# Kernel optimization log

Measured on AMD Instinct MI355X. Metric: run time of the kernel, lower is better.

The kernel has to match this reference:

```python
import jax, jax.numpy as jnp
import numpy as np

B, S, D, H = 2, 2048, 1024, 16
DEPTH = D // H


def setup_inputs() -> dict:
    key = jax.random.key(0)
    ks = jax.random.split(key, 12)
    s = 0.02
    inp = {
        "query": jax.random.normal(ks[0], (B, S, D), jnp.float32),
        "key": jax.random.normal(ks[1], (B, S, D), jnp.float32),
        "value": jax.random.normal(ks[2], (B, S, D), jnp.float32),
        # causal mask: 1.0 where attention is disallowed (j > i)
        "mask": jnp.triu(jnp.ones((S, S), jnp.float32), k=1)[None, None, :, :],
        "wq": jax.random.normal(ks[3], (D, D), jnp.float32) * s,
        "bq": jnp.zeros((D,), jnp.float32),
        "wk": jax.random.normal(ks[4], (D, D), jnp.float32) * s,
        "bk": jnp.zeros((D,), jnp.float32),
        "wv": jax.random.normal(ks[5], (D, D), jnp.float32) * s,
        "bv": jnp.zeros((D,), jnp.float32),
        "wo": jax.random.normal(ks[6], (D, D), jnp.float32) * s,
        "bo": jnp.zeros((D,), jnp.float32),
    }
    return inp


def _split_heads(x):
    # [B,S,D] -> [B,H,S,depth]
    b, s, _ = x.shape
    return x.reshape(b, s, H, DEPTH).transpose(0, 2, 1, 3)


def reference(query, key, value, mask, wq, bq, wk, bk, wv, bv, wo, bo):
    q = _split_heads(query @ wq + bq)
    k = _split_heads(key @ wk + bk)
    v = _split_heads(value @ wv + bv)
    scale = jnp.sqrt(jnp.asarray(DEPTH, jnp.float32))
    scores = jnp.einsum("bhqd,bhkd->bhqk", q, k) / scale  # [B,H,S,S]
    scores = scores + mask * (-1e9)
    attn = jax.nn.softmax(scores, axis=-1)
    out = jnp.einsum("bhqk,bhkd->bhqd", attn, v)
    out = out.transpose(0, 2, 1, 3).reshape(query.shape[0], query.shape[1], D)
    return out @ wo + bo
```

## Files before the change

### kernel.cpp

```cpp
#include <hip/hip_runtime.h>
#include <hip/hip_bf16.h>
#include <stdint.h>
#include <math.h>

typedef float f32x4  __attribute__((ext_vector_type(4)));
typedef float f32x16 __attribute__((ext_vector_type(16)));
typedef short s16x8  __attribute__((ext_vector_type(8)));
typedef unsigned u32x4 __attribute__((ext_vector_type(4)));

#define SEQ     2048
#define DMODEL  1024
#define MROWS   4096
#define NHEAD   16

__device__ __forceinline__ unsigned short f2b(float x) {
    union { float f; unsigned u; } un; un.f = x;
    unsigned r = un.u + 0x7FFFu + ((un.u >> 16) & 1u);
    return (unsigned short)(r >> 16);
}

__device__ __forceinline__ unsigned cvtpk(float lo, float hi_) {
    unsigned r;
    asm("v_cvt_pk_bf16_f32 %0, %1, %2" : "=v"(r) : "v"(lo), "v"(hi_));
    return r;
}

#define EXP2(x) __builtin_amdgcn_exp2f(x)

__device__ __forceinline__ void g2l16(const void* g, void* l) {
    __builtin_amdgcn_global_load_lds(
        (const __attribute__((address_space(1))) unsigned int*)g,
        (__attribute__((address_space(3))) unsigned int*)l,
        16, 0, 0);
}

__global__ __launch_bounds__(256) void cvt3_kernel(
    const float* __restrict__ q, const float* __restrict__ k, const float* __restrict__ v,
    unsigned short* __restrict__ out)
{
    const float* in = blockIdx.y == 0 ? q : (blockIdx.y == 1 ? k : v);
    size_t i = ((size_t)blockIdx.x * 256 + threadIdx.x) * 4;
    float4 val = *(const float4*)(in + i);
    ushort4 o;
    o.x = f2b(val.x); o.y = f2b(val.y); o.z = f2b(val.z); o.w = f2b(val.w);
    *(ushort4*)(out + (size_t)blockIdx.y * ((size_t)MROWS * DMODEL) + i) = o;
}

__global__ __launch_bounds__(256) void wtrans_kernel(
    const float* __restrict__ w0, const float* __restrict__ w1,
    const float* __restrict__ w2, const float* __restrict__ w3,
    unsigned short* __restrict__ wt)
{
    const int z = blockIdx.z;
    const float* w = z == 0 ? w0 : z == 1 ? w1 : z == 2 ? w2 : w3;
    __shared__ float t[32][33];
    const int bx = blockIdx.x * 32;
    const int by = blockIdx.y * 32;
    const int tx = threadIdx.x, ty = threadIdx.y;
    #pragma unroll
    for (int i = 0; i < 4; ++i)
        t[ty + i*8][tx] = w[(size_t)(by + ty + i*8) * DMODEL + bx + tx];
    __syncthreads();
    unsigned short* o = wt + (size_t)z * ((size_t)DMODEL * DMODEL);
    #pragma unroll
    for (int i = 0; i < 4; ++i) {
        int nrel = ty + i*8, krel = tx;
        o[(size_t)(bx + nrel) * DMODEL + by + krel] = f2b(t[krel][nrel]);
    }
}

template<int TM>
__global__ __launch_bounds__(256, (TM == 128 ? 3 : 2)) void gemm_kernel(
    int mode_base,
    const unsigned short* __restrict__ xbase,
    const unsigned short* __restrict__ wtbase,
    const float* __restrict__ b0, const float* __restrict__ b1,
    const float* __restrict__ b2, const float* __restrict__ b3,
    unsigned short* __restrict__ qh, unsigned short* __restrict__ kh,
    unsigned short* __restrict__ vT, float* __restrict__ outF)
{
    constexpr int WM = TM / 2;
    constexpr int MT = WM / 16;
    const int mode = mode_base + blockIdx.z;
    const unsigned short* Ap = xbase + (size_t)(mode < 3 ? mode : 0) * ((size_t)MROWS * DMODEL);
    const unsigned short* Bt = wtbase + (size_t)mode * ((size_t)DMODEL * DMODEL);
    const float* bias = mode == 0 ? b0 : mode == 1 ? b1 : mode == 2 ? b2 : b3;

    __shared__ unsigned short As[TM * 64];
    __shared__ unsigned short Bs[128 * 64];

    const int tid = threadIdx.x;
    const int lane = tid & 63, wid = tid >> 6;
    const int ll = lane & 15, lg = lane >> 4;
    const int mb = blockIdx.x * TM, nb = blockIdx.y * 128;
    const int wr = wid >> 1, wc = wid & 1;

    f32x4 acc[MT][4] = {};

    for (int kb = 0; kb < DMODEL; kb += 64) {
        __syncthreads();
        #pragma unroll
        for (int is = 0; is < TM / 32; ++is) {
            int ci = is * 256 + tid;
            int r = ci >> 3;
            int cbs = ((ci & 7) * 16) ^ ((r & 7) << 4);
            g2l16((const char*)Ap + ((size_t)(mb + r) * DMODEL + kb) * 2 + cbs,
                  (char*)As + (is * 256 + wid * 64) * 16);
        }
        #pragma unroll
        for (int is = 0; is < 4; ++is) {
            int ci = is * 256 + tid;
            int r = ci >> 3;
            int cbs = ((ci & 7) * 16) ^ ((r & 7) << 4);
            g2l16((const char*)Bt + ((size_t)(nb + r) * DMODEL + kb) * 2 + cbs,
                  (char*)Bs + (is * 256 + wid * 64) * 16);
        }
        __syncthreads();
        #pragma unroll
        for (int kk = 0; kk < 2; ++kk) {
            s16x8 af[MT], bfr[4];
            #pragma unroll
            for (int m = 0; m < MT; ++m) {
                int row = wr * WM + m * 16 + ll;
                int cbyte = (kk * 64 + lg * 16) ^ ((row & 7) << 4);
                af[m] = *(const s16x8*)((const char*)As + row * 128 + cbyte);
            }
            #pragma unroll
            for (int n = 0; n < 4; ++n) {
                int row = wc * 64 + n * 16 + ll;
                int cbyte = (kk * 64 + lg * 16) ^ ((row & 7) << 4);
                bfr[n] = *(const s16x8*)((const char*)Bs + row * 128 + cbyte);
            }
            #pragma unroll
            for (int m = 0; m < MT; ++m)
                #pragma unroll
                for (int n = 0; n < 4; ++n)
                    acc[m][n] = __builtin_amdgcn_mfma_f32_16x16x32_bf16(af[m], bfr[n], acc[m][n], 0, 0, 0);
        }
    }

    #pragma unroll
    for (int m = 0; m < MT; ++m) {
        int grow0 = mb + wr * WM + m * 16 + lg * 4;
        #pragma unroll
        for (int n = 0; n < 4; ++n) {
            int col = nb + wc * 64 + n * 16 + ll;
            float bc = bias[col];
            f32x4 v = acc[m][n];
            if (mode == 3) {
                #pragma unroll
                for (int r = 0; r < 4; ++r)
                    outF[(size_t)(grow0 + r) * DMODEL + col] = v[r] + bc;
            } else if (mode == 2) {
                int b = grow0 >> 11, s0 = grow0 & 2047;
                int h = col >> 6, d = col & 63;
                ushort4 pk;
                pk.x = f2b(v[0] + bc); pk.y = f2b(v[1] + bc);
                pk.z = f2b(v[2] + bc); pk.w = f2b(v[3] + bc);
                *(ushort4*)(vT + ((size_t)((b * NHEAD + h) * 64 + d) << 11) + s0) = pk;
            } else {
                unsigned short* dst = (mode == 0) ? qh : kh;
                float scl = (mode == 0) ? 0.125f * 1.44269504089f : 1.0f;
                int b = grow0 >> 11, s0 = grow0 & 2047;
                int h = col >> 6, d = col & 63;
                #pragma unroll
                for (int r = 0; r < 4; ++r)
                    dst[((size_t)(b * NHEAD + h) * SEQ + s0 + r) * 64 + d] = f2b((v[r] + bc) * scl);
            }
        }
    }
}

__global__ __launch_bounds__(256, 2) void attn_kernel(
    const unsigned short* __restrict__ qh, const unsigned short* __restrict__ kh,
    const unsigned short* __restrict__ vT, unsigned short* __restrict__ attnout)
{
    const int bh = blockIdx.x;
    const int t = blockIdx.y;
    const int qb = t * 128;
    const int nsteps = 2 * t + 2;

    const unsigned short* Q = qh + (size_t)bh * (SEQ * 64);
    const unsigned short* K = kh + (size_t)bh * (SEQ * 64);
    const unsigned short* V = vT + (size_t)bh * (64 * SEQ);

    __shared__ unsigned short Ks[2][64 * 64];
    __shared__ unsigned short Vs[2][64 * 64];
    __shared__ float lsc[128];

    const int tid = threadIdx.x, lane = tid & 63, wid = tid >> 6;
    const int l31 = lane & 31, hi = lane >> 5;
    const int qrow = qb + wid * 32 + l31;
    const int smax = 2 * t + (wid >> 1);
    const int swz = (l31 & 7) << 4;

    const int sr0 = tid >> 3;
    const int sb0 = ((tid & 7) * 16) ^ ((sr0 & 7) << 4);
    const int sr1 = (tid + 256) >> 3;
    const int sb1 = ((tid & 7) * 16) ^ ((sr1 & 7) << 4);

    s16x8 aq[4];
    {
        const unsigned short* qp = Q + (size_t)qrow * 64 + hi * 8;
        #pragma unroll
        for (int u = 0; u < 4; ++u)
            aq[u] = *(const s16x8*)(qp + u * 16);
    }

    f32x16 oc0 = {}, oc1 = {};
    float mrow = -1e30f, lrow = 0.f;

    g2l16((const char*)K + ((size_t)sr0 * 64) * 2 + sb0, (char*)Ks[0] + (wid * 64) * 16);
    g2l16((const char*)K + ((size_t)sr1 * 64) * 2 + sb1, (char*)Ks[0] + (256 + wid * 64) * 16);
    g2l16((const char*)V + ((size_t)sr0 * SEQ) * 2 + sb0, (char*)Vs[0] + (wid * 64) * 16);
    g2l16((const char*)V + ((size_t)sr1 * SEQ) * 2 + sb1, (char*)Vs[0] + (256 + wid * 64) * 16);
    __syncthreads();

    int cur = 0;
    for (int step = 0; step < nsteps; ++step) {
        const int kb = step * 64;
        if (step + 1 < nsteps) {
            const int kn = kb + 64;
            g2l16((const char*)K + ((size_t)(kn + sr0) * 64) * 2 + sb0, (char*)Ks[cur ^ 1] + (wid * 64) * 16);
            g2l16((const char*)K + ((size_t)(kn + sr1) * 64) * 2 + sb1, (char*)Ks[cur ^ 1] + (256 + wid * 64) * 16);
            g2l16((const char*)V + ((size_t)sr0 * SEQ + kn) * 2 + sb0, (char*)Vs[cur ^ 1] + (wid * 64) * 16);
            g2l16((const char*)V + ((size_t)sr1 * SEQ + kn) * 2 + sb1, (char*)Vs[cur ^ 1] + (256 + wid * 64) * 16);
        }
        if (step <= smax) {
            const char* KsC = (const char*)Ks[cur];
            const char* VsC = (const char*)Vs[cur];

            f32x16 p0 = {}, p1 = {};
            __builtin_amdgcn_s_setprio(1);
            #pragma unroll
            for (int u = 0; u < 4; ++u) {
                int cb = (u * 32 + hi * 16) ^ swz;
                s16x8 k0 = *(const s16x8*)(KsC + l31 * 128 + cb);
                s16x8 k1 = *(const s16x8*)(KsC + (32 + l31) * 128 + cb);
                p0 = __builtin_amdgcn_mfma_f32_32x32x16_bf16(k0, aq[u], p0, 0, 0, 0);
                p1 = __builtin_amdgcn_mfma_f32_32x32x16_bf16(k1, aq[u], p1, 0, 0, 0);
            }
            __builtin_amdgcn_s_setprio(0);

            if (step == smax) {
                #pragma unroll
                for (int r = 0; r < 16; ++r) {
                    int rl = (r & 3) + 8 * (r >> 2) + 4 * hi;
                    if (kb + rl > qrow)      p0[r] = -1e30f;
                    if (kb + 32 + rl > qrow) p1[r] = -1e30f;
                }
            }

            float tm[8];
            #pragma unroll
            for (int i = 0; i < 8; ++i)
                tm[i] = fmaxf(fmaxf(p0[i], p0[i + 8]), fmaxf(p1[i], p1[i + 8]));
            float mx = fmaxf(fmaxf(fmaxf(tm[0], tm[1]), fmaxf(tm[2], tm[3])),
                             fmaxf(fmaxf(tm[4], tm[5]), fmaxf(tm[6], tm[7])));
            mx = fmaxf(mx, __shfl_xor(mx, 32, 64));

            if (!__all(mx - mrow <= 8.0f)) {
                float mnew = fmaxf(mrow, mx);
                float sclf = EXP2(mrow - mnew);
                lrow *= sclf;
                #pragma unroll
                for (int r = 0; r < 16; ++r) {
                    int src = (r & 3) + 8 * (r >> 2) + 4 * hi;
                    float sf = __shfl(sclf, src, 64);
                    oc0[r] *= sf;
                    oc1[r] *= sf;
                }
                mrow = mnew;
            }

            #pragma unroll
            for (int i = 0; i < 16; ++i) { p0[i] = EXP2(p0[i] - mrow); p1[i] = EXP2(p1[i] - mrow); }

            float s8[8];
            #pragma unroll
            for (int i = 0; i < 8; ++i)
                s8[i] = (p0[i] + p0[i + 8]) + (p1[i] + p1[i + 8]);
            float ts = ((s8[0] + s8[1]) + (s8[2] + s8[3])) + ((s8[4] + s8[5]) + (s8[6] + s8[7]));
            ts += __shfl_xor(ts, 32, 64);
            lrow += ts;

            s16x8 pa[4];
            #pragma unroll
            for (int g = 0; g < 4; ++g) {
                const f32x16 pv = (g < 2) ? p0 : p1;
                const int o = (g & 1) * 8;
                unsigned c01 = cvtpk(pv[o + 0], pv[o + 1]);
                unsigned c23 = cvtpk(pv[o + 2], pv[o + 3]);
                unsigned c45 = cvtpk(pv[o + 4], pv[o + 5]);
                unsigned c67 = cvtpk(pv[o + 6], pv[o + 7]);
                unsigned c01x = (unsigned)__shfl_xor((int)c01, 32, 64);
                unsigned c23x = (unsigned)__shfl_xor((int)c23, 32, 64);
                unsigned c45x = (unsigned)__shfl_xor((int)c45, 32, 64);
                unsigned c67x = (unsigned)__shfl_xor((int)c67, 32, 64);
                unsigned w0 = hi ? c45x : c01;
                unsigned w1 = hi ? c67x : c23;
                unsigned w2 = hi ? c45  : c01x;
                unsigned w3 = hi ? c67  : c23x;
                u32x4 t4 = {w0, w1, w2, w3};
                pa[g] = __builtin_bit_cast(s16x8, t4);
            }

            __builtin_amdgcn_s_setprio(1);
            #pragma unroll
            for (int s = 0; s < 4; ++s) {
                int cb = (s * 32 + hi * 16) ^ swz;
                s16x8 vb0 = *(const s16x8*)(VsC + l31 * 128 + cb);
                s16x8 vb1 = *(const s16x8*)(VsC + (32 + l31) * 128 + cb);
                oc0 = __builtin_amdgcn_mfma_f32_32x32x16_bf16(pa[s], vb0, oc0, 0, 0, 0);
                oc1 = __builtin_amdgcn_mfma_f32_32x32x16_bf16(pa[s], vb1, oc1, 0, 0, 0);
            }
            __builtin_amdgcn_s_setprio(0);
        }
        __syncthreads();
        cur ^= 1;
    }

    float inv = 1.0f / lrow;
    if (hi == 0) lsc[wid * 32 + l31] = inv;
    const int b = bh >> 4, h = bh & 15;
    #pragma unroll
    for (int r = 0; r < 16; ++r) {
        int rl = (r & 3) + 8 * (r >> 2) + 4 * hi;
        float li = lsc[wid * 32 + rl];
        size_t base = ((size_t)(b * SEQ + qb + wid * 32 + rl) << 10) + h * 64;
        attnout[base + l31]      = f2b(oc0[r] * li);
        attnout[base + 32 + l31] = f2b(oc1[r] * li);
    }
}

extern "C" void kernel_launch(void* const* d_in, const int* in_sizes, int n_in,
                              void* d_out, int out_size, void* d_ws, size_t ws_size,
                              hipStream_t stream) {
    const float* query = (const float*)d_in[0];
    const float* key   = (const float*)d_in[1];
    const float* value = (const float*)d_in[2];
    const float* wq = (const float*)d_in[4];
    const float* bq = (const float*)d_in[5];
    const float* wk = (const float*)d_in[6];
    const float* bk = (const float*)d_in[7];
    const float* wv = (const float*)d_in[8];
    const float* bv = (const float*)d_in[9];
    const float* wo = (const float*)d_in[10];
    const float* bo = (const float*)d_in[11];
    float* out = (float*)d_out;

    char* ws = (char*)d_ws;
    unsigned short* xb  = (unsigned short*)ws;
    unsigned short* wt  = (unsigned short*)(ws + 25165824);
    unsigned short* qhp = (unsigned short*)(ws + 33554432);
    unsigned short* khp = (unsigned short*)(ws + 41943040);
    unsigned short* vTp = (unsigned short*)(ws + 50331648);

    cvt3_kernel<<<dim3(4096, 3), 256, 0, stream>>>(query, key, value, xb);
    wtrans_kernel<<<dim3(32, 32, 4), dim3(32, 8), 0, stream>>>(wq, wk, wv, wo, wt);
    gemm_kernel<128><<<dim3(32, 8, 3), 256, 0, stream>>>(0, xb, wt, bq, bk, bv, bo, qhp, khp, vTp, nullptr);
    attn_kernel<<<dim3(32, 16), 256, 0, stream>>>(qhp, khp, vTp, xb);
    gemm_kernel<64><<<dim3(64, 8, 1), 256, 0, stream>>>(3, xb, wt, bq, bk, bv, bo, qhp, khp, vTp, out);
}
```

Before: 116.5 us.

## Restructure attention into single-wave blocks reading K/V directly from global

The attention kernel now runs one 64-thread wave per block, each handling 32 query rows, with 2048 blocks ordered heaviest causal tiles first. The shared-memory double buffering and block barriers are gone, and K and V fragments are loaded straight from global memory (relying on cache) into the MFMA operands. This removes synchronisation and idle waves in causal tail steps and improves load balance. The cost is redundant global/L2 traffic, since each wave refetches K/V tiles without sharing them across the waves of a block.

Measured after the change: 153.6 us. 31.8% more time.

```diff
diff --git a/kernel.cpp b/kernel.cpp
--- a/kernel.cpp
+++ b/kernel.cpp
@@ -171,33 +171,24 @@
     }
 }
 
-__global__ __launch_bounds__(256, 2) void attn_kernel(
+__global__ __launch_bounds__(64, 4) void attn_kernel(
     const unsigned short* __restrict__ qh, const unsigned short* __restrict__ kh,
     const unsigned short* __restrict__ vT, unsigned short* __restrict__ attnout)
 {
-    const int bh = blockIdx.x;
-    const int t = blockIdx.y;
-    const int qb = t * 128;
-    const int nsteps = 2 * t + 2;
+    const int bx = blockIdx.x;
+    const int bh = bx & 31;
+    const int j  = 63 - (bx >> 5);
+    const int qb = j * 32;
+    const int smax = j >> 1;
+    const int nsteps = smax + 1;
 
     const unsigned short* Q = qh + (size_t)bh * (SEQ * 64);
     const unsigned short* K = kh + (size_t)bh * (SEQ * 64);
     const unsigned short* V = vT + (size_t)bh * (64 * SEQ);
 
-    __shared__ unsigned short Ks[2][64 * 64];
-    __shared__ unsigned short Vs[2][64 * 64];
-    __shared__ float lsc[128];
-
-    const int tid = threadIdx.x, lane = tid & 63, wid = tid >> 6;
+    const int lane = threadIdx.x;
     const int l31 = lane & 31, hi = lane >> 5;
-    const int qrow = qb + wid * 32 + l31;
-    const int smax = 2 * t + (wid >> 1);
-    const int swz = (l31 & 7) << 4;
-
-    const int sr0 = tid >> 3;
-    const int sb0 = ((tid & 7) * 16) ^ ((sr0 & 7) << 4);
-    const int sr1 = (tid + 256) >> 3;
-    const int sb1 = ((tid & 7) * 16) ^ ((sr1 & 7) << 4);
+    const int qrow = qb + l31;
 
     s16x8 aq[4];
     {
@@ -210,124 +201,101 @@
     f32x16 oc0 = {}, oc1 = {};
     float mrow = -1e30f, lrow = 0.f;
 
-    g2l16((const char*)K + ((size_t)sr0 * 64) * 2 + sb0, (char*)Ks[0] + (wid * 64) * 16);
-    g2l16((const char*)K + ((size_t)sr1 * 64) * 2 + sb1, (char*)Ks[0] + (256 + wid * 64) * 16);
-    g2l16((const char*)V + ((size_t)sr0 * SEQ) * 2 + sb0, (char*)Vs[0] + (wid * 64) * 16);
-    g2l16((const char*)V + ((size_t)sr1 * SEQ) * 2 + sb1, (char*)Vs[0] + (256 + wid * 64) * 16);
-    __syncthreads();
-
-    int cur = 0;
+    const unsigned short* Vrow = V + (size_t)l31 * SEQ + hi * 8;
+
     for (int step = 0; step < nsteps; ++step) {
         const int kb = step * 64;
-        if (step + 1 < nsteps) {
-            const int kn = kb + 64;
-            g2l16((const char*)K + ((size_t)(kn + sr0) * 64) * 2 + sb0, (char*)Ks[cur ^ 1] + (wid * 64) * 16);
-            g2l16((const char*)K + ((size_t)(kn + sr1) * 64) * 2 + sb1, (char*)Ks[cur ^ 1] + (256 + wid * 64) * 16);
-            g2l16((const char*)V + ((size_t)sr0 * SEQ + kn) * 2 + sb0, (char*)Vs[cur ^ 1] + (wid * 64) * 16);
-            g2l16((const char*)V + ((size_t)sr1 * SEQ + kn) * 2 + sb1, (char*)Vs[cur ^ 1] + (256 + wid * 64) * 16);
-        }
-        if (step <= smax) {
-            const char* KsC = (const char*)Ks[cur];
-            const char* VsC = (const char*)Vs[cur];
-
-            f32x16 p0 = {}, p1 = {};
+
+        const unsigned short* Kp = K + ((size_t)(kb + l31)) * 64 + hi * 8;
+        f32x16 p0 = {}, p1 = {};
+        __builtin_amdgcn_s_setprio(1);
+        #pragma unroll
+        for (int u = 0; u < 4; ++u) {
+            s16x8 k0 = *(const s16x8*)(Kp + u * 16);
+            s16x8 k1 = *(const s16x8*)(Kp + 32 * 64 + u * 16);
+            p0 = __builtin_amdgcn_mfma_f32_32x32x16_bf16(k0, aq[u], p0, 0, 0, 0);
+            p1 = __builtin_amdgcn_mfma_f32_32x32x16_bf16(k1, aq[u], p1, 0, 0, 0);
+        }
+        __builtin_amdgcn_s_setprio(0);
+
+        if (step == smax) {
+            #pragma unroll
+            for (int r = 0; r < 16; ++r) {
+                int rl = (r & 3) + 8 * (r >> 2) + 4 * hi;
+                if (kb + rl > qrow)      p0[r] = -1e30f;
+                if (kb + 32 + rl > qrow) p1[r] = -1e30f;
+            }
+        }
+
+        float tm[8];
+        #pragma unroll
+        for (int i = 0; i < 8; ++i)
+            tm[i] = fmaxf(fmaxf(p0[i], p0[i + 8]), fmaxf(p1[i], p1[i + 8]));
+        float mx = fmaxf(fmaxf(fmaxf(tm[0], tm[1]), fmaxf(tm[2], tm[3])),
+                         fmaxf(fmaxf(tm[4], tm[5]), fmaxf(tm[6], tm[7])));
+        mx = fmaxf(mx, __shfl_xor(mx, 32, 64));
+
+        if (!__all(mx - mrow <= 8.0f)) {
+            float mnew = fmaxf(mrow, mx);
+            float sclf = EXP2(mrow - mnew);
+            lrow *= sclf;
+            #pragma unroll
+            for (int r = 0; r < 16; ++r) {
+                int src = (r & 3) + 8 * (r >> 2) + 4 * hi;
+                float sf = __shfl(sclf, src, 64);
+                oc0[r] *= sf;
+                oc1[r] *= sf;
+            }
+            mrow = mnew;
+        }
+
+        #pragma unroll
+        for (int i = 0; i < 16; ++i) { p0[i] = EXP2(p0[i] - mrow); p1[i] = EXP2(p1[i] - mrow); }
+
+        float s8[8];
+        #pragma unroll
+        for (int i = 0; i < 8; ++i)
+            s8[i] = (p0[i] + p0[i + 8]) + (p1[i] + p1[i + 8]);
+        float ts = ((s8[0] + s8[1]) + (s8[2] + s8[3])) + ((s8[4] + s8[5]) + (s8[6] + s8[7]));
+        ts += __shfl_xor(ts, 32, 64);
+        lrow += ts;
+
+        const unsigned short* Vp = Vrow + kb;
+        #pragma unroll
+        for (int g = 0; g < 4; ++g) {
+            const f32x16 pv = (g < 2) ? p0 : p1;
+            const int o = (g & 1) * 8;
+            unsigned c01 = cvtpk(pv[o + 0], pv[o + 1]);
+            unsigned c23 = cvtpk(pv[o + 2], pv[o + 3]);
+            unsigned c45 = cvtpk(pv[o + 4], pv[o + 5]);
+            unsigned c67 = cvtpk(pv[o + 6], pv[o + 7]);
+            unsigned c01x = (unsigned)__shfl_xor((int)c01, 32, 64);
+            unsigned c23x = (unsigned)__shfl_xor((int)c23, 32, 64);
+            unsigned c45x = (unsigned)__shfl_xor((int)c45, 32, 64);
+            unsigned c67x = (unsigned)__shfl_xor((int)c67, 32, 64);
+            unsigned w0 = hi ? c45x : c01;
+            unsigned w1 = hi ? c67x : c23;
+            unsigned w2 = hi ? c45  : c01x;
+            unsigned w3 = hi ? c67  : c23x;
+            u32x4 t4 = {w0, w1, w2, w3};
+            s16x8 pa = __builtin_bit_cast(s16x8, t4);
+
+            s16x8 vb0 = *(const s16x8*)(Vp + g * 16);
+            s16x8 vb1 = *(const s16x8*)(Vp + 32 * SEQ + g * 16);
             __builtin_amdgcn_s_setprio(1);
-            #pragma unroll
-            for (int u = 0; u < 4; ++u) {
-                int cb = (u * 32 + hi * 16) ^ swz;
-                s16x8 k0 = *(const s16x8*)(KsC + l31 * 128 + cb);
-                s16x8 k1 = *(const s16x8*)(KsC + (32 + l31) * 128 + cb);
-                p0 = __builtin_amdgcn_mfma_f32_32x32x16_bf16(k0, aq[u], p0, 0, 0, 0);
-                p1 = __builtin_amdgcn_mfma_f32_32x32x16_bf16(k1, aq[u], p1, 0, 0, 0);
-            }
+            oc0 = __builtin_amdgcn_mfma_f32_32x32x16_bf16(pa, vb0, oc0, 0, 0, 0);
+            oc1 = __builtin_amdgcn_mfma_f32_32x32x16_bf16(pa, vb1, oc1, 0, 0, 0);
             __builtin_amdgcn_s_setprio(0);
-
-            if (step == smax) {
-                #pragma unroll
-                for (int r = 0; r < 16; ++r) {
-                    int rl = (r & 3) + 8 * (r >> 2) + 4 * hi;
-                    if (kb + rl > qrow)      p0[r] = -1e30f;
-                    if (kb + 32 + rl > qrow) p1[r] = -1e30f;
-                }
-            }
-
-            float tm[8];
-            #pragma unroll
-            for (int i = 0; i < 8; ++i)
-                tm[i] = fmaxf(fmaxf(p0[i], p0[i + 8]), fmaxf(p1[i], p1[i + 8]));
-            float mx = fmaxf(fmaxf(fmaxf(tm[0], tm[1]), fmaxf(tm[2], tm[3])),
-                             fmaxf(fmaxf(tm[4], tm[5]), fmaxf(tm[6], tm[7])));
-            mx = fmaxf(mx, __shfl_xor(mx, 32, 64));
-
-            if (!__all(mx - mrow <= 8.0f)) {
-                float mnew = fmaxf(mrow, mx);
-                float sclf = EXP2(mrow - mnew);
-                lrow *= sclf;
-                #pragma unroll
-                for (int r = 0; r < 16; ++r) {
-                    int src = (r & 3) + 8 * (r >> 2) + 4 * hi;
-                    float sf = __shfl(sclf, src, 64);
-                    oc0[r] *= sf;
-                    oc1[r] *= sf;
-                }
-                mrow = mnew;
-            }
-
-            #pragma unroll
-            for (int i = 0; i < 16; ++i) { p0[i] = EXP2(p0[i] - mrow); p1[i] = EXP2(p1[i] - mrow); }
-
-            float s8[8];
-            #pragma unroll
-            for (int i = 0; i < 8; ++i)
-                s8[i] = (p0[i] + p0[i + 8]) + (p1[i] + p1[i + 8]);
-            float ts = ((s8[0] + s8[1]) + (s8[2] + s8[3])) + ((s8[4] + s8[5]) + (s8[6] + s8[7]));
-            ts += __shfl_xor(ts, 32, 64);
-            lrow += ts;
-
-            s16x8 pa[4];
-            #pragma unroll
-            for (int g = 0; g < 4; ++g) {
-                const f32x16 pv = (g < 2) ? p0 : p1;
-                const int o = (g & 1) * 8;
-                unsigned c01 = cvtpk(pv[o + 0], pv[o + 1]);
-                unsigned c23 = cvtpk(pv[o + 2], pv[o + 3]);
-                unsigned c45 = cvtpk(pv[o + 4], pv[o + 5]);
-                unsigned c67 = cvtpk(pv[o + 6], pv[o + 7]);
-                unsigned c01x = (unsigned)__shfl_xor((int)c01, 32, 64);
-                unsigned c23x = (unsigned)__shfl_xor((int)c23, 32, 64);
-                unsigned c45x = (unsigned)__shfl_xor((int)c45, 32, 64);
-                unsigned c67x = (unsigned)__shfl_xor((int)c67, 32, 64);
-                unsigned w0 = hi ? c45x : c01;
-                unsigned w1 = hi ? c67x : c23;
-                unsigned w2 = hi ? c45  : c01x;
-                unsigned w3 = hi ? c67  : c23x;
-                u32x4 t4 = {w0, w1, w2, w3};
-                pa[g] = __builtin_bit_cast(s16x8, t4);
-            }
-
-            __builtin_amdgcn_s_setprio(1);
-            #pragma unroll
-            for (int s = 0; s < 4; ++s) {
-                int cb = (s * 32 + hi * 16) ^ swz;
-                s16x8 vb0 = *(const s16x8*)(VsC + l31 * 128 + cb);
-                s16x8 vb1 = *(const s16x8*)(VsC + (32 + l31) * 128 + cb);
-                oc0 = __builtin_amdgcn_mfma_f32_32x32x16_bf16(pa[s], vb0, oc0, 0, 0, 0);
-                oc1 = __builtin_amdgcn_mfma_f32_32x32x16_bf16(pa[s], vb1, oc1, 0, 0, 0);
-            }
-            __builtin_amdgcn_s_setprio(0);
-        }
-        __syncthreads();
-        cur ^= 1;
+        }
     }
 
     float inv = 1.0f / lrow;
-    if (hi == 0) lsc[wid * 32 + l31] = inv;
     const int b = bh >> 4, h = bh & 15;
     #pragma unroll
     for (int r = 0; r < 16; ++r) {
         int rl = (r & 3) + 8 * (r >> 2) + 4 * hi;
-        float li = lsc[wid * 32 + rl];
-        size_t base = ((size_t)(b * SEQ + qb + wid * 32 + rl) << 10) + h * 64;
+        float li = __shfl(inv, rl, 64);
+        size_t base = ((size_t)(b * SEQ + qb + rl) << 10) + h * 64;
         attnout[base + l31]      = f2b(oc0[r] * li);
         attnout[base + 32 + l31] = f2b(oc1[r] * li);
     }
@@ -359,6 +327,6 @@
     cvt3_kernel<<<dim3(4096, 3), 256, 0, stream>>>(query, key, value, xb);
     wtrans_kernel<<<dim3(32, 32, 4), dim3(32, 8), 0, stream>>>(wq, wk, wv, wo, wt);
     gemm_kernel<128><<<dim3(32, 8, 3), 256, 0, stream>>>(0, xb, wt, bq, bk, bv, bo, qhp, khp, vTp, nullptr);
-    attn_kernel<<<dim3(32, 16), 256, 0, stream>>>(qhp, khp, vTp, xb);
+    attn_kernel<<<dim3(2048), 64, 0, stream>>>(qhp, khp, vTp, xb);
     gemm_kernel<64><<<dim3(64, 8, 1), 256, 0, stream>>>(3, xb, wt, bq, bk, bv, bo, qhp, khp, vTp, out);
 }
```

## Shrink attention blocks to 64 query rows and schedule longest causal tiles first

Applied to the files above, without the earlier changes.

Attention blocks now hold 2 waves covering 64 query rows instead of 4 waves covering 128. The launch is a 1D grid of 1024 blocks ordered so the longest causal rows run first, which is meant to balance the triangular workload and drop per-wave idle steps. The lane-half exchange when packing probabilities to bf16 now uses v_permlane32_swap instead of shuffles plus selects. The trade-off is that each K/V tile loaded into LDS is shared by only two waves, so global-to-LDS traffic per unit of work doubles.

Measured after the change: 111.5 us. 1.04x faster.

```diff
diff --git a/kernel.cpp b/kernel.cpp
--- a/kernel.cpp
+++ b/kernel.cpp
@@ -171,14 +171,15 @@
     }
 }
 
-__global__ __launch_bounds__(256, 2) void attn_kernel(
+__global__ __launch_bounds__(128, 2) void attn_kernel(
     const unsigned short* __restrict__ qh, const unsigned short* __restrict__ kh,
     const unsigned short* __restrict__ vT, unsigned short* __restrict__ attnout)
 {
-    const int bh = blockIdx.x;
-    const int t = blockIdx.y;
-    const int qb = t * 128;
-    const int nsteps = 2 * t + 2;
+    const int bid = blockIdx.x;
+    const int bh = bid & 31;
+    const int j  = 31 - (bid >> 5);
+    const int qb = j * 64;
+    const int nsteps = j + 1;
 
     const unsigned short* Q = qh + (size_t)bh * (SEQ * 64);
     const unsigned short* K = kh + (size_t)bh * (SEQ * 64);
@@ -186,18 +187,12 @@
 
     __shared__ unsigned short Ks[2][64 * 64];
     __shared__ unsigned short Vs[2][64 * 64];
-    __shared__ float lsc[128];
+    __shared__ float lsc[64];
 
     const int tid = threadIdx.x, lane = tid & 63, wid = tid >> 6;
     const int l31 = lane & 31, hi = lane >> 5;
     const int qrow = qb + wid * 32 + l31;
-    const int smax = 2 * t + (wid >> 1);
     const int swz = (l31 & 7) << 4;
-
-    const int sr0 = tid >> 3;
-    const int sb0 = ((tid & 7) * 16) ^ ((sr0 & 7) << 4);
-    const int sr1 = (tid + 256) >> 3;
-    const int sb1 = ((tid & 7) * 16) ^ ((sr1 & 7) << 4);
 
     s16x8 aq[4];
     {
@@ -210,115 +205,115 @@
     f32x16 oc0 = {}, oc1 = {};
     float mrow = -1e30f, lrow = 0.f;
 
-    g2l16((const char*)K + ((size_t)sr0 * 64) * 2 + sb0, (char*)Ks[0] + (wid * 64) * 16);
-    g2l16((const char*)K + ((size_t)sr1 * 64) * 2 + sb1, (char*)Ks[0] + (256 + wid * 64) * 16);
-    g2l16((const char*)V + ((size_t)sr0 * SEQ) * 2 + sb0, (char*)Vs[0] + (wid * 64) * 16);
-    g2l16((const char*)V + ((size_t)sr1 * SEQ) * 2 + sb1, (char*)Vs[0] + (256 + wid * 64) * 16);
+#define STAGE(KDST, VDST, KB)                                                            \
+    {                                                                                    \
+        _Pragma("unroll")                                                                \
+        for (int it = 0; it < 4; ++it) {                                                 \
+            int ci = it * 128 + tid;                                                     \
+            int sr = ci >> 3;                                                            \
+            int sb = ((ci & 7) * 16) ^ ((sr & 7) << 4);                                  \
+            int lb = (it * 128 + wid * 64) * 16;                                         \
+            g2l16((const char*)K + ((size_t)((KB) + sr) * 64) * 2 + sb, (char*)(KDST) + lb); \
+            g2l16((const char*)V + ((size_t)sr * SEQ + (KB)) * 2 + sb, (char*)(VDST) + lb); \
+        }                                                                                \
+    }
+
+    STAGE(Ks[0], Vs[0], 0);
     __syncthreads();
 
     int cur = 0;
     for (int step = 0; step < nsteps; ++step) {
         const int kb = step * 64;
-        if (step + 1 < nsteps) {
-            const int kn = kb + 64;
-            g2l16((const char*)K + ((size_t)(kn + sr0) * 64) * 2 + sb0, (char*)Ks[cur ^ 1] + (wid * 64) * 16);
-            g2l16((const char*)K + ((size_t)(kn + sr1) * 64) * 2 + sb1, (char*)Ks[cur ^ 1] + (256 + wid * 64) * 16);
-            g2l16((const char*)V + ((size_t)sr0 * SEQ + kn) * 2 + sb0, (char*)Vs[cur ^ 1] + (wid * 64) * 16);
-            g2l16((const char*)V + ((size_t)sr1 * SEQ + kn) * 2 + sb1, (char*)Vs[cur ^ 1] + (256 + wid * 64) * 16);
-        }
-        if (step <= smax) {
-            const char* KsC = (const char*)Ks[cur];
-            const char* VsC = (const char*)Vs[cur];
-
-            f32x16 p0 = {}, p1 = {};
-            __builtin_amdgcn_s_setprio(1);
-            #pragma unroll
-            for (int u = 0; u < 4; ++u) {
-                int cb = (u * 32 + hi * 16) ^ swz;
-                s16x8 k0 = *(const s16x8*)(KsC + l31 * 128 + cb);
-                s16x8 k1 = *(const s16x8*)(KsC + (32 + l31) * 128 + cb);
-                p0 = __builtin_amdgcn_mfma_f32_32x32x16_bf16(k0, aq[u], p0, 0, 0, 0);
-                p1 = __builtin_amdgcn_mfma_f32_32x32x16_bf16(k1, aq[u], p1, 0, 0, 0);
-            }
-            __builtin_amdgcn_s_setprio(0);
-
-            if (step == smax) {
-                #pragma unroll
-                for (int r = 0; r < 16; ++r) {
-                    int rl = (r & 3) + 8 * (r >> 2) + 4 * hi;
-                    if (kb + rl > qrow)      p0[r] = -1e30f;
-                    if (kb + 32 + rl > qrow) p1[r] = -1e30f;
-                }
-            }
-
-            float tm[8];
-            #pragma unroll
-            for (int i = 0; i < 8; ++i)
-                tm[i] = fmaxf(fmaxf(p0[i], p0[i + 8]), fmaxf(p1[i], p1[i + 8]));
-            float mx = fmaxf(fmaxf(fmaxf(tm[0], tm[1]), fmaxf(tm[2], tm[3])),
-                             fmaxf(fmaxf(tm[4], tm[5]), fmaxf(tm[6], tm[7])));
-            mx = fmaxf(mx, __shfl_xor(mx, 32, 64));
-
-            if (!__all(mx - mrow <= 8.0f)) {
-                float mnew = fmaxf(mrow, mx);
-                float sclf = EXP2(mrow - mnew);
-                lrow *= sclf;
-                #pragma unroll
-                for (int r = 0; r < 16; ++r) {
-                    int src = (r & 3) + 8 * (r >> 2) + 4 * hi;
-                    float sf = __shfl(sclf, src, 64);
-                    oc0[r] *= sf;
-                    oc1[r] *= sf;
-                }
-                mrow = mnew;
-            }
-
-            #pragma unroll
-            for (int i = 0; i < 16; ++i) { p0[i] = EXP2(p0[i] - mrow); p1[i] = EXP2(p1[i] - mrow); }
-
-            float s8[8];
-            #pragma unroll
-            for (int i = 0; i < 8; ++i)
-                s8[i] = (p0[i] + p0[i + 8]) + (p1[i] + p1[i + 8]);
-            float ts = ((s8[0] + s8[1]) + (s8[2] + s8[3])) + ((s8[4] + s8[5]) + (s8[6] + s8[7]));
-            ts += __shfl_xor(ts, 32, 64);
-            lrow += ts;
-
-            s16x8 pa[4];
-            #pragma unroll
-            for (int g = 0; g < 4; ++g) {
-                const f32x16 pv = (g < 2) ? p0 : p1;
-                const int o = (g & 1) * 8;
-                unsigned c01 = cvtpk(pv[o + 0], pv[o + 1]);
-                unsigned c23 = cvtpk(pv[o + 2], pv[o + 3]);
-                unsigned c45 = cvtpk(pv[o + 4], pv[o + 5]);
-                unsigned c67 = cvtpk(pv[o + 6], pv[o + 7]);
-                unsigned c01x = (unsigned)__shfl_xor((int)c01, 32, 64);
-                unsigned c23x = (unsigned)__shfl_xor((int)c23, 32, 64);
-                unsigned c45x = (unsigned)__shfl_xor((int)c45, 32, 64);
-                unsigned c67x = (unsigned)__shfl_xor((int)c67, 32, 64);
-                unsigned w0 = hi ? c45x : c01;
-                unsigned w1 = hi ? c67x : c23;
-                unsigned w2 = hi ? c45  : c01x;
-                unsigned w3 = hi ? c67  : c23x;
-                u32x4 t4 = {w0, w1, w2, w3};
-                pa[g] = __builtin_bit_cast(s16x8, t4);
-            }
-
-            __builtin_amdgcn_s_setprio(1);
-            #pragma unroll
-            for (int s = 0; s < 4; ++s) {
-                int cb = (s * 32 + hi * 16) ^ swz;
-                s16x8 vb0 = *(const s16x8*)(VsC + l31 * 128 + cb);
-                s16x8 vb1 = *(const s16x8*)(VsC + (32 + l31) * 128 + cb);
-                oc0 = __builtin_amdgcn_mfma_f32_32x32x16_bf16(pa[s], vb0, oc0, 0, 0, 0);
-                oc1 = __builtin_amdgcn_mfma_f32_32x32x16_bf16(pa[s], vb1, oc1, 0, 0, 0);
-            }
-            __builtin_amdgcn_s_setprio(0);
-        }
+        if (step + 1 < nsteps)
+            STAGE(Ks[cur ^ 1], Vs[cur ^ 1], kb + 64);
+
+        const char* KsC = (const char*)Ks[cur];
+        const char* VsC = (const char*)Vs[cur];
+
+        f32x16 p0 = {}, p1 = {};
+        __builtin_amdgcn_s_setprio(1);
+        #pragma unroll
+        for (int u = 0; u < 4; ++u) {
+            int cb = (u * 32 + hi * 16) ^ swz;
+            s16x8 k0 = *(const s16x8*)(KsC + l31 * 128 + cb);
+            s16x8 k1 = *(const s16x8*)(KsC + (32 + l31) * 128 + cb);
+            p0 = __builtin_amdgcn_mfma_f32_32x32x16_bf16(k0, aq[u], p0, 0, 0, 0);
+            p1 = __builtin_amdgcn_mfma_f32_32x32x16_bf16(k1, aq[u], p1, 0, 0, 0);
+        }
+        __builtin_amdgcn_s_setprio(0);
+
+        if (step == nsteps - 1) {
+            #pragma unroll
+            for (int r = 0; r < 16; ++r) {
+                int rl = (r & 3) + 8 * (r >> 2) + 4 * hi;
+                if (kb + rl > qrow)      p0[r] = -1e30f;
+                if (kb + 32 + rl > qrow) p1[r] = -1e30f;
+            }
+        }
+
+        float tm[8];
+        #pragma unroll
+        for (int i = 0; i < 8; ++i)
+            tm[i] = fmaxf(fmaxf(p0[i], p0[i + 8]), fmaxf(p1[i], p1[i + 8]));
+        float mx = fmaxf(fmaxf(fmaxf(tm[0], tm[1]), fmaxf(tm[2], tm[3])),
+                         fmaxf(fmaxf(tm[4], tm[5]), fmaxf(tm[6], tm[7])));
+        mx = fmaxf(mx, __shfl_xor(mx, 32, 64));
+
+        if (!__all(mx - mrow <= 8.0f)) {
+            float mnew = fmaxf(mrow, mx);
+            float sclf = EXP2(mrow - mnew);
+            lrow *= sclf;
+            #pragma unroll
+            for (int r = 0; r < 16; ++r) {
+                int src = (r & 3) + 8 * (r >> 2) + 4 * hi;
+                float sf = __shfl(sclf, src, 64);
+                oc0[r] *= sf;
+                oc1[r] *= sf;
+            }
+            mrow = mnew;
+        }
+
+        #pragma unroll
+        for (int i = 0; i < 16; ++i) { p0[i] = EXP2(p0[i] - mrow); p1[i] = EXP2(p1[i] - mrow); }
+
+        float s8[8];
+        #pragma unroll
+        for (int i = 0; i < 8; ++i)
+            s8[i] = (p0[i] + p0[i + 8]) + (p1[i] + p1[i + 8]);
+        float ts = ((s8[0] + s8[1]) + (s8[2] + s8[3])) + ((s8[4] + s8[5]) + (s8[6] + s8[7]));
+        ts += __shfl_xor(ts, 32, 64);
+        lrow += ts;
+
+        s16x8 pa[4];
+        #pragma unroll
+        for (int g = 0; g < 4; ++g) {
+            const f32x16 pv = (g < 2) ? p0 : p1;
+            const int o = (g & 1) * 8;
+            unsigned a0 = cvtpk(pv[o + 0], pv[o + 1]);
+            unsigned a1 = cvtpk(pv[o + 2], pv[o + 3]);
+            unsigned b0 = cvtpk(pv[o + 4], pv[o + 5]);
+            unsigned b1 = cvtpk(pv[o + 6], pv[o + 7]);
+            asm("v_permlane32_swap_b32 %0, %1" : "+v"(a0), "+v"(b0));
+            asm("v_permlane32_swap_b32 %0, %1" : "+v"(a1), "+v"(b1));
+            u32x4 t4 = {a0, a1, b0, b1};
+            pa[g] = __builtin_bit_cast(s16x8, t4);
+        }
+
+        __builtin_amdgcn_s_setprio(1);
+        #pragma unroll
+        for (int s = 0; s < 4; ++s) {
+            int cb = (s * 32 + hi * 16) ^ swz;
+            s16x8 vb0 = *(const s16x8*)(VsC + l31 * 128 + cb);
+            s16x8 vb1 = *(const s16x8*)(VsC + (32 + l31) * 128 + cb);
+            oc0 = __builtin_amdgcn_mfma_f32_32x32x16_bf16(pa[s], vb0, oc0, 0, 0, 0);
+            oc1 = __builtin_amdgcn_mfma_f32_32x32x16_bf16(pa[s], vb1, oc1, 0, 0, 0);
+        }
+        __builtin_amdgcn_s_setprio(0);
+
         __syncthreads();
         cur ^= 1;
     }
+#undef STAGE
 
     float inv = 1.0f / lrow;
     if (hi == 0) lsc[wid * 32 + l31] = inv;
@@ -359,6 +354,6 @@
     cvt3_kernel<<<dim3(4096, 3), 256, 0, stream>>>(query, key, value, xb);
     wtrans_kernel<<<dim3(32, 32, 4), dim3(32, 8), 0, stream>>>(wq, wk, wv, wo, wt);
     gemm_kernel<128><<<dim3(32, 8, 3), 256, 0, stream>>>(0, xb, wt, bq, bk, bv, bo, qhp, khp, vTp, nullptr);
-    attn_kernel<<<dim3(32, 16), 256, 0, stream>>>(qhp, khp, vTp, xb);
+    attn_kernel<<<dim3(1024), 128, 0, stream>>>(qhp, khp, vTp, xb);
     gemm_kernel<64><<<dim3(64, 8, 1), 256, 0, stream>>>(3, xb, wt, bq, bk, bv, bo, qhp, khp, vTp, out);
 }
```
